# Kernel tuning notes

Hardware: AMD Instinct MI355X
Metric: run time of the kernel (lower is better)

The kernel has to match this reference:

```python
import jax, jax.numpy as jnp
import numpy as np

B, S, D, H, OUT = 512, 200, 64, 512, 1
EPS = 1e-5  # torch LayerNorm default


def ln(x, g, b, axes=-1):
    m = x.mean(axis=axes, keepdims=True)
    v = ((x - m) ** 2).mean(axis=axes, keepdims=True)
    return (x - m) * jax.lax.rsqrt(v + EPS) * g + b


def lstm_layer(xs, W_ih, b_ih, W_hh, b_hh, g_ih, be_ih, g_hh, be_hh, g_ho, be_ho):
    # xs: (S, B, in_dim) -> (S, B, H)
    nb = xs.shape[1]
    def step(carry, x_t):
        h, c = carry
        gates = ln(x_t @ W_ih.T + b_ih, g_ih, be_ih) + ln(h @ W_hh.T + b_hh, g_hh, be_hh)
        i, f, g, o = jnp.split(gates, 4, axis=-1)
        c_new = jax.nn.sigmoid(f) * c + jax.nn.sigmoid(i) * jnp.tanh(g)
        h_new = jax.nn.sigmoid(o) * ln(jnp.tanh(c_new), g_ho, be_ho)
        return (h_new, c_new), h_new
    init = (jnp.zeros((nb, H), xs.dtype), jnp.zeros((nb, H), xs.dtype))
    _, hs = jax.lax.scan(step, init, xs)
    return hs


def setup_inputs() -> dict:
    key = jax.random.key(0)
    ks = iter(jax.random.split(key, 16))
    scale = 0.02
    def rn(shape):
        return jax.random.normal(next(ks), shape, jnp.float32) * scale
    inp = {"x": jax.random.normal(next(ks), (B, S, D), jnp.float32)}
    inp["ln1_g"] = jnp.ones((S, D), jnp.float32)
    inp["ln1_b"] = jnp.zeros((S, D), jnp.float32)
    for l, ind in ((0, D), (1, H)):
        inp[f"W_ih{l}"] = rn((4 * H, ind)); inp[f"b_ih{l}"] = jnp.zeros((4 * H,), jnp.float32)
        inp[f"W_hh{l}"] = rn((4 * H, H));  inp[f"b_hh{l}"] = jnp.zeros((4 * H,), jnp.float32)
        inp[f"g_ih{l}"] = jnp.ones((4 * H,), jnp.float32); inp[f"be_ih{l}"] = jnp.zeros((4 * H,), jnp.float32)
        inp[f"g_hh{l}"] = jnp.ones((4 * H,), jnp.float32); inp[f"be_hh{l}"] = jnp.zeros((4 * H,), jnp.float32)
        inp[f"g_ho{l}"] = jnp.ones((H,), jnp.float32);     inp[f"be_ho{l}"] = jnp.zeros((H,), jnp.float32)
    inp["Wd1"] = rn((H // 4, H));      inp["bd1"] = jnp.zeros((H // 4,), jnp.float32)
    inp["Wd2"] = rn((H // 8, H // 4)); inp["bd2"] = jnp.zeros((H // 8,), jnp.float32)
    inp["Wd3"] = rn((H // 16, H // 8)); inp["bd3"] = jnp.zeros((H // 16,), jnp.float32)
    inp["Wd4"] = rn((OUT, H // 16));   inp["bd4"] = jnp.zeros((OUT,), jnp.float32)
    return inp


def _forward(x, ln1_g, ln1_b,
             W_ih0, b_ih0, W_hh0, b_hh0, g_ih0, be_ih0, g_hh0, be_hh0, g_ho0, be_ho0,
             W_ih1, b_ih1, W_hh1, b_hh1, g_ih1, be_ih1, g_hh1, be_hh1, g_ho1, be_ho1,
             Wd1, bd1, Wd2, bd2, Wd3, bd3, Wd4, bd4):
    # ln1 normalizes jointly over (seq_len, input_dim)
    x = ln(x, ln1_g, ln1_b, axes=(-2, -1))
    xs = jnp.transpose(x, (1, 0, 2))  # (S, B, D)
    hs = lstm_layer(xs, W_ih0, b_ih0, W_hh0, b_hh0, g_ih0, be_ih0, g_hh0, be_hh0, g_ho0, be_ho0)
    hs = lstm_layer(hs, W_ih1, b_ih1, W_hh1, b_hh1, g_ih1, be_ih1, g_hh1, be_hh1, g_ho1, be_ho1)
    h_last = hs[-1]  # (B, H): last_num=1, eval-mode dropout is identity
    z = jax.nn.relu(h_last @ Wd1.T + bd1)
    z = jax.nn.relu(z @ Wd2.T + bd2)
    z = jax.nn.relu(z @ Wd3.T + bd3)
    return z @ Wd4.T + bd4  # (B, OUT)


def reference(x, ln1_g, ln1_b,
              W_ih0, b_ih0, W_hh0, b_hh0, g_ih0, be_ih0, g_hh0, be_hh0, g_ho0, be_ho0,
              W_ih1, b_ih1, W_hh1, b_hh1, g_ih1, be_ih1, g_hh1, be_hh1, g_ho1, be_ho1,
              Wd1, bd1, Wd2, bd2, Wd3, bd3, Wd4, bd4):
    return _forward(x, ln1_g, ln1_b,
                    W_ih0, b_ih0, W_hh0, b_hh0, g_ih0, be_ih0, g_hh0, be_hh0, g_ho0, be_ho0,
                    W_ih1, b_ih1, W_hh1, b_hh1, g_ih1, be_ih1, g_hh1, be_hh1, g_ho1, be_ho1,
                    Wd1, bd1, Wd2, bd2, Wd3, bd3, Wd4, bd4)
```

## Files before the change

kernel.cpp:

```cpp
#include <hip/hip_runtime.h>
#include <math.h>

#define BATCH 512
#define SEQ   200
#define DIN   64
#define HID   512
#define GW    2048
#define EPS   1e-5f
#define NREG  4

typedef _Float16 half_t;
typedef half_t half8 __attribute__((ext_vector_type(8)));
typedef float  f32x4  __attribute__((ext_vector_type(4)));
typedef float  f32x16 __attribute__((ext_vector_type(16)));

#define WN0 (2048*64)
#define WN1 (2048*512)
#define WTOT (WN0 + 3*WN1)
#define XFRAG ((size_t)SEQ*16*4*512)

__device__ __forceinline__ float sigf(float x){ return 1.0f/(1.0f+expf(-x)); }

__device__ __forceinline__ void block_reduce4(float&a,float&b,float&c,float&d,float* red){
  #pragma unroll
  for(int o=32;o;o>>=1){
    a+=__shfl_down(a,o); b+=__shfl_down(b,o);
    c+=__shfl_down(c,o); d+=__shfl_down(d,o);
  }
  const int lane = threadIdx.x & 63, wid = threadIdx.x>>6;
  if(lane==0){ red[wid*4+0]=a; red[wid*4+1]=b; red[wid*4+2]=c; red[wid*4+3]=d; }
  __syncthreads();
  a = red[0]+red[4]+red[8]+red[12];
  b = red[1]+red[5]+red[9]+red[13];
  c = red[2]+red[6]+red[10]+red[14];
  d = red[3]+red[7]+red[11]+red[15];
  __syncthreads();
}

__global__ __launch_bounds__(256) void ln1_stats(const float* __restrict__ x,
                                                 float* __restrict__ mu,
                                                 float* __restrict__ rs){
  const int b = blockIdx.x;
  const float* xb = x + (size_t)b*SEQ*DIN;
  float s=0, ss=0, d=0, e=0;
  for (int i=threadIdx.x; i<SEQ*DIN; i+=256){ float v=xb[i]; s+=v; ss+=v*v; }
  __shared__ float red[16];
  block_reduce4(s,ss,d,e,red);
  if (threadIdx.x==0){
    float m = s*(1.0f/(SEQ*DIN));
    mu[b] = m;
    rs[b] = rsqrtf(ss*(1.0f/(SEQ*DIN)) - m*m + EPS);
  }
}

__global__ __launch_bounds__(256) void wsplit(
    const float* __restrict__ W0, const float* __restrict__ W1,
    const float* __restrict__ W2, const float* __restrict__ W3,
    half_t* __restrict__ Wh, half_t* __restrict__ Wl)
{
  int i = blockIdx.x*256 + threadIdx.x;
  if (i >= WTOT) return;
  const float* src; int off, Kd;
  if (i < WN0){ src=W0; off=i; Kd=DIN; }
  else {
    int r = (i-WN0)/WN1; off = (i-WN0) - r*WN1; Kd=HID;
    src = (r==0)?W1:((r==1)?W2:W3);
  }
  const int C = Kd>>5;
  int j  = off & 7;
  int l  = (off>>3) & 63;
  int ks = (off>>9) & 1;
  int nf = (off>>10) & 1;
  int pc = off>>11;
  int c  = pc & (C-1);
  int p  = pc >> (Kd==DIN ? 1 : 4);
  int n  = p*64 + nf*32 + (l&31);
  int k  = c*32 + ks*16 + (l>>5)*8 + j;
  float v = src[(size_t)n*Kd + k];
  half_t h = (half_t)v;
  Wh[i] = h;
  Wl[i] = (half_t)(v - (float)h);
}

__global__ __launch_bounds__(256) void xprep(
    const float* __restrict__ x, const float* __restrict__ g1, const float* __restrict__ b1,
    const float* __restrict__ mu, const float* __restrict__ rs,
    half_t* __restrict__ xh, half_t* __restrict__ xl)
{
  size_t i = (size_t)blockIdx.x*256 + threadIdx.x;
  if (i >= XFRAG) return;
  int j   = (int)(i & 7);
  int l   = (int)((i>>3) & 63);
  int c   = (int)((i>>9) & 3);
  int mch = (int)((i>>11) & 15);
  int t   = (int)(i>>15);
  int b   = mch*32 + (l&31);
  int k   = c*16 + ((l>>5)<<3) + j;
  float v = (x[(size_t)b*(SEQ*DIN) + t*DIN + k] - mu[b]) * rs[b]
            * g1[t*DIN+k] + b1[t*DIN+k];
  half_t h = (half_t)v;
  xh[i] = h;
  xl[i] = (half_t)(v - (float)h);
}

__global__ __launch_bounds__(256, 1) void tick_mm64(
    const half_t* __restrict__ xh, const half_t* __restrict__ xl,
    const half_t* __restrict__ h0fh, const half_t* __restrict__ h0fl,
    const half_t* __restrict__ h1fh, const half_t* __restrict__ h1fl,
    const half_t* __restrict__ Wh, const half_t* __restrict__ Wl,
    float* __restrict__ G, int t)
{
  const int bi   = blockIdx.x;
  const int xcd  = bi & 7;
  const int slot = bi >> 3;
  const int z    = slot & 3;
  const int y    = (slot >> 2) & 3;
  const int x    = xcd*2 + (slot >> 4);

  const int tid  = threadIdx.x;
  const int lane = tid & 63;
  const int w    = tid >> 6;
  const int ln31 = lane & 31;

  const int mch0 = y*4 + (w>>1)*2;
  const int p    = x*2 + (w&1);
  const int wn0  = p*64;

  const half_t* Bh = Wh + WN0; const half_t* Bl = Wl + WN0;
  int Kd = HID;
  if (z==0){ Bh=Wh; Bl=Wl; Kd=DIN; }
  else if (z==2){ Bh=Wh+WN0+WN1; Bl=Wl+WN0+WN1; }
  else if (z==3){ Bh=Wh+WN0+2*WN1; Bl=Wl+WN0+2*WN1; }

  const int C32 = Kd >> 5;
  const int C16 = Kd >> 4;

  const half_t* Bph = Bh + (size_t)p*C32*2048 + lane*8;
  const half_t* Bpl = Bl + (size_t)p*C32*2048 + lane*8;

  const int tq = (t < SEQ) ? t : (SEQ-1);
  const half_t *Aph0,*Apl0,*Aph1,*Apl1;
  if (z==0){
    const size_t xb = ((size_t)tq*16 + mch0)*2048 + lane*8;
    Aph0 = xh + xb; Aph1 = xh + xb + 2048;
    Apl0 = xl + xb; Apl1 = xl + xb + 2048;
  } else {
    const half_t* FAh = (z==3) ? h1fh : h0fh;
    const half_t* FAl = (z==3) ? h1fl : h0fl;
    const size_t ab = (size_t)mch0*16384 + lane*8;
    Aph0 = FAh + ab; Aph1 = FAh + ab + 16384;
    Apl0 = FAl + ab; Apl1 = FAl + ab + 16384;
  }

  f32x16 acc00 = {0.f,0.f,0.f,0.f,0.f,0.f,0.f,0.f,0.f,0.f,0.f,0.f,0.f,0.f,0.f,0.f};
  f32x16 acc01 = acc00, acc10 = acc00, acc11 = acc00;

  struct F { half8 ah0,al0,ah1,al1,bh0,bh1,bl0,bl1; };
  auto loadF = [&](int c)->F{
    F f;
    const size_t ao = (size_t)c*512;
    f.ah0 = *(const half8*)(Aph0 + ao);
    f.al0 = *(const half8*)(Apl0 + ao);
    f.ah1 = *(const half8*)(Aph1 + ao);
    f.al1 = *(const half8*)(Apl1 + ao);
    const size_t bo = (size_t)(c>>1)*2048 + (size_t)(c&1)*512;
    f.bh0 = *(const half8*)(Bph + bo);
    f.bh1 = *(const half8*)(Bph + bo + 1024);
    f.bl0 = *(const half8*)(Bpl + bo);
    f.bl1 = *(const half8*)(Bpl + bo + 1024);
    return f;
  };
  auto mmstep = [&](const F& f){
    acc00 = __builtin_amdgcn_mfma_f32_32x32x16_f16(f.ah0, f.bh0, acc00, 0,0,0);
    acc01 = __builtin_amdgcn_mfma_f32_32x32x16_f16(f.ah0, f.bh1, acc01, 0,0,0);
    acc10 = __builtin_amdgcn_mfma_f32_32x32x16_f16(f.ah1, f.bh0, acc10, 0,0,0);
    acc11 = __builtin_amdgcn_mfma_f32_32x32x16_f16(f.ah1, f.bh1, acc11, 0,0,0);
    acc00 = __builtin_amdgcn_mfma_f32_32x32x16_f16(f.al0, f.bh0, acc00, 0,0,0);
    acc01 = __builtin_amdgcn_mfma_f32_32x32x16_f16(f.al0, f.bh1, acc01, 0,0,0);
    acc10 = __builtin_amdgcn_mfma_f32_32x32x16_f16(f.al1, f.bh0, acc10, 0,0,0);
    acc11 = __builtin_amdgcn_mfma_f32_32x32x16_f16(f.al1, f.bh1, acc11, 0,0,0);
    acc00 = __builtin_amdgcn_mfma_f32_32x32x16_f16(f.ah0, f.bl0, acc00, 0,0,0);
    acc01 = __builtin_amdgcn_mfma_f32_32x32x16_f16(f.ah0, f.bl1, acc01, 0,0,0);
    acc10 = __builtin_amdgcn_mfma_f32_32x32x16_f16(f.ah1, f.bl0, acc10, 0,0,0);
    acc11 = __builtin_amdgcn_mfma_f32_32x32x16_f16(f.ah1, f.bl1, acc11, 0,0,0);
  };

  F f0 = loadF(0);
  F f1 = loadF(1);
  for (int c=0; c<C16; c+=2){
    F f2, f3;
    if (c+2 < C16){ f2 = loadF(c+2); f3 = loadF(c+3); }
    mmstep(f0);
    mmstep(f1);
    f0 = f2; f1 = f3;
  }

  float* Gr = G + (size_t)z*BATCH*GW;
  const int rbase = (lane>>5)<<2;
  #pragma unroll
  for (int reg=0; reg<16; reg++){
    const int row = (reg&3) + ((reg>>2)<<3) + rbase;
    const int m0 = mch0*32 + row;
    const int m1 = m0 + 32;
    __builtin_nontemporal_store(acc00[reg], &Gr[(size_t)m0*GW + wn0 + ln31]);
    __builtin_nontemporal_store(acc01[reg], &Gr[(size_t)m0*GW + wn0 + 32 + ln31]);
    __builtin_nontemporal_store(acc10[reg], &Gr[(size_t)m1*GW + wn0 + ln31]);
    __builtin_nontemporal_store(acc11[reg], &Gr[(size_t)m1*GW + wn0 + 32 + ln31]);
  }
}

__global__ __launch_bounds__(256) void tick_update(
    const float* __restrict__ G,
    const float* __restrict__ b_ih0, const float* __restrict__ b_hh0,
    const float* __restrict__ b_ih1, const float* __restrict__ b_hh1,
    const float* __restrict__ g_ih0, const float* __restrict__ be_ih0,
    const float* __restrict__ g_hh0, const float* __restrict__ be_hh0,
    const float* __restrict__ g_ho0, const float* __restrict__ be_ho0,
    const float* __restrict__ g_ih1, const float* __restrict__ be_ih1,
    const float* __restrict__ g_hh1, const float* __restrict__ be_hh1,
    const float* __restrict__ g_ho1, const float* __restrict__ be_ho1,
    float* __restrict__ h0, float* __restrict__ c0,
    float* __restrict__ h1, float* __restrict__ c1,
    half_t* __restrict__ h0fh, half_t* __restrict__ h0fl,
    half_t* __restrict__ h1fh, half_t* __restrict__ h1fl, int t)
{
  const int layer = blockIdx.x >> 9;
  const int b = blockIdx.x & 511;
  if (layer==0 && t>=SEQ) return;
  if (layer==1 && t==0)   return;

  const float *GA,*GB,*bA,*bB,*gA,*beA,*gB,*beB,*gH,*bH;
  float *cs,*hs; half_t *hfx,*lfx;
  const size_t rb = (size_t)b*GW;
  if (layer==0){
    GA = G + rb;
    GB = G + (size_t)1*BATCH*GW + rb;
    bA=b_ih0; bB=b_hh0;
    gA=g_ih0; beA=be_ih0; gB=g_hh0; beB=be_hh0; gH=g_ho0; bH=be_ho0;
    cs = c0 + b*HID; hs = nullptr; hfx = h0fh; lfx = h0fl;
  } else {
    GA = G + (size_t)2*BATCH*GW + rb;
    GB = G + (size_t)3*BATCH*GW + rb;
    bA=b_ih1; bB=b_hh1;
    gA=g_ih1; beA=be_ih1; gB=g_hh1; beB=be_hh1; gH=g_ho1; bH=be_ho1;
    cs = c1 + b*HID; hs = (t==SEQ) ? (h1 + b*HID) : nullptr; hfx = h1fh; lfx = h1fl;
  }

  const int tid = threadIdx.x;
  __shared__ float red[16];
  __shared__ __align__(16) float GS[2*GW];
  __shared__ float su[HID];
  __shared__ float so[HID];

  float sa=0, ssa=0, sb=0, ssb=0;
  for (int i=tid*4; i<GW; i+=1024){
    f32x4 va = __builtin_nontemporal_load((const f32x4*)(GA+i));
    va += *(const f32x4*)(bA+i);
    *(f32x4*)(GS+i) = va;
    f32x4 vb = __builtin_nontemporal_load((const f32x4*)(GB+i));
    vb += *(const f32x4*)(bB+i);
    *(f32x4*)(GS+GW+i) = vb;
    #pragma unroll
    for (int q=0;q<4;q++){
      sa += va[q]; ssa += va[q]*va[q];
      sb += vb[q]; ssb += vb[q]*vb[q];
    }
  }
  block_reduce4(sa,ssa,sb,ssb,red);
  const float ma = sa*(1.0f/GW);
  const float ra = rsqrtf(ssa*(1.0f/GW) - ma*ma + EPS);
  const float mb = sb*(1.0f/GW);
  const float rb_ = rsqrtf(ssb*(1.0f/GW) - mb*mb + EPS);

  float s_u=0, s_uu=0;
  for (int j=tid;j<HID;j+=256){
    float iv = ((GS[j      ]-ma)*ra*gA[j      ]+beA[j      ]) + ((GS[GW+j      ]-mb)*rb_*gB[j      ]+beB[j      ]);
    float fv = ((GS[j+  HID]-ma)*ra*gA[j+  HID]+beA[j+  HID]) + ((GS[GW+j+  HID]-mb)*rb_*gB[j+  HID]+beB[j+  HID]);
    float gv = ((GS[j+2*HID]-ma)*ra*gA[j+2*HID]+beA[j+2*HID]) + ((GS[GW+j+2*HID]-mb)*rb_*gB[j+2*HID]+beB[j+2*HID]);
    float ov = ((GS[j+3*HID]-ma)*ra*gA[j+3*HID]+beA[j+3*HID]) + ((GS[GW+j+3*HID]-mb)*rb_*gB[j+3*HID]+beB[j+3*HID]);
    float cn = sigf(fv)*cs[j] + sigf(iv)*tanhf(gv);
    cs[j] = cn;
    float u = tanhf(cn);
    su[j] = u; so[j] = sigf(ov);
    s_u += u; s_uu += u*u;
  }
  float d3=0,d4=0;
  block_reduce4(s_u,s_uu,d3,d4,red);
  const float mu_u = s_u*(1.0f/HID);
  const float ru   = rsqrtf(s_uu*(1.0f/HID) - mu_u*mu_u + EPS);

  const size_t fbase = ((size_t)(b>>5)*32)*512 + (size_t)(b&31)*8;
  for (int j=tid;j<HID;j+=256){
    float v = so[j] * ((su[j]-mu_u)*ru*gH[j] + bH[j]);
    if (hs) hs[j] = v;
    half_t hv = (half_t)v;
    half_t lv = (half_t)(v - (float)hv);
    const size_t fi = fbase + (size_t)(j>>4)*512 + (size_t)((j>>3)&1)*256 + (j&7);
    hfx[fi] = hv;
    lfx[fi] = lv;
  }
}

__global__ __launch_bounds__(256) void head_kernel(
    const float* __restrict__ h1,
    const float* __restrict__ Wd1, const float* __restrict__ bd1,
    const float* __restrict__ Wd2, const float* __restrict__ bd2,
    const float* __restrict__ Wd3, const float* __restrict__ bd3,
    const float* __restrict__ Wd4, const float* __restrict__ bd4,
    float* __restrict__ out)
{
  const int b = blockIdx.x;
  __shared__ float hv[HID];
  __shared__ float z1[128];
  __shared__ float z2[64];
  __shared__ float z3[32];
  const int tid = threadIdx.x;
  for (int i=tid;i<HID;i+=256) hv[i]=h1[(size_t)b*HID+i];
  __syncthreads();
  if (tid<128){
    float acc=bd1[tid]; const float* w=Wd1+(size_t)tid*512;
    for(int k=0;k<512;k++) acc+=hv[k]*w[k];
    z1[tid]=fmaxf(acc,0.f);
  }
  __syncthreads();
  if (tid<64){
    float acc=bd2[tid]; const float* w=Wd2+(size_t)tid*128;
    for(int k=0;k<128;k++) acc+=z1[k]*w[k];
    z2[tid]=fmaxf(acc,0.f);
  }
  __syncthreads();
  if (tid<32){
    float acc=bd3[tid]; const float* w=Wd3+(size_t)tid*64;
    for(int k=0;k<64;k++) acc+=z2[k]*w[k];
    z3[tid]=fmaxf(acc,0.f);
  }
  __syncthreads();
  if (tid==0){
    float acc=bd4[0];
    for(int k=0;k<32;k++) acc+=z3[k]*Wd4[k];
    out[b]=acc;
  }
}

extern "C" void kernel_launch(void* const* d_in, const int* in_sizes, int n_in,
                              void* d_out, int out_size, void* d_ws, size_t ws_size,
                              hipStream_t stream) {
  const float* x      = (const float*)d_in[0];
  const float* ln1_g  = (const float*)d_in[1];
  const float* ln1_b  = (const float*)d_in[2];
  const float* W_ih0  = (const float*)d_in[3];
  const float* b_ih0  = (const float*)d_in[4];
  const float* W_hh0  = (const float*)d_in[5];
  const float* b_hh0  = (const float*)d_in[6];
  const float* g_ih0  = (const float*)d_in[7];
  const float* be_ih0 = (const float*)d_in[8];
  const float* g_hh0  = (const float*)d_in[9];
  const float* be_hh0 = (const float*)d_in[10];
  const float* g_ho0  = (const float*)d_in[11];
  const float* be_ho0 = (const float*)d_in[12];
  const float* W_ih1  = (const float*)d_in[13];
  const float* b_ih1  = (const float*)d_in[14];
  const float* W_hh1  = (const float*)d_in[15];
  const float* b_hh1  = (const float*)d_in[16];
  const float* g_ih1  = (const float*)d_in[17];
  const float* be_ih1 = (const float*)d_in[18];
  const float* g_hh1  = (const float*)d_in[19];
  const float* be_hh1 = (const float*)d_in[20];
  const float* g_ho1  = (const float*)d_in[21];
  const float* be_ho1 = (const float*)d_in[22];
  const float* Wd1    = (const float*)d_in[23];
  const float* bd1    = (const float*)d_in[24];
  const float* Wd2    = (const float*)d_in[25];
  const float* bd2    = (const float*)d_in[26];
  const float* Wd3    = (const float*)d_in[27];
  const float* bd3    = (const float*)d_in[28];
  const float* Wd4    = (const float*)d_in[29];
  const float* bd4    = (const float*)d_in[30];
  float* out = (float*)d_out;

  float* ws = (float*)d_ws;
  float* G  = ws;
  float* h0 = G  + NREG*(size_t)BATCH*GW;
  float* c0 = h0 + (size_t)BATCH*HID;
  float* h1 = c0 + (size_t)BATCH*HID;
  float* c1 = h1 + (size_t)BATCH*HID;
  half_t* h0fh = (half_t*)(c1 + (size_t)BATCH*HID);
  half_t* h0fl = h0fh + (size_t)BATCH*HID;
  half_t* h1fh = h0fl + (size_t)BATCH*HID;
  half_t* h1fl = h1fh + (size_t)BATCH*HID;
  float* mu = (float*)(h1fl + (size_t)BATCH*HID);
  float* rs = mu + BATCH;
  half_t* Wh = (half_t*)(rs + BATCH);
  half_t* Wl = Wh + (size_t)WTOT;
  half_t* xh = Wl + (size_t)WTOT;
  half_t* xl = xh + XFRAG;

  (void)hipMemsetAsync(h0, 0, 4*(size_t)BATCH*HID*4 + 4*(size_t)BATCH*HID*2, stream);

  ln1_stats<<<BATCH, 256, 0, stream>>>(x, mu, rs);
  wsplit<<<(WTOT+255)/256, 256, 0, stream>>>(W_ih0, W_hh0, W_ih1, W_hh1, Wh, Wl);
  xprep<<<(int)((XFRAG+255)/256), 256, 0, stream>>>(x, ln1_g, ln1_b, mu, rs, xh, xl);

  for (int t = 0; t <= SEQ; ++t) {
    tick_mm64<<<dim3(256), 256, 0, stream>>>(xh, xl,
        h0fh, h0fl, h1fh, h1fl, Wh, Wl, G, t);
    tick_update<<<dim3(1024), 256, 0, stream>>>(G,
        b_ih0, b_hh0, b_ih1, b_hh1,
        g_ih0, be_ih0, g_hh0, be_hh0, g_ho0, be_ho0,
        g_ih1, be_ih1, g_hh1, be_hh1, g_ho1, be_ho1,
        h0, c0, h1, c1, h0fh, h0fl, h1fh, h1fl, t);
  }
  head_kernel<<<BATCH, 256, 0, stream>>>(h1, Wd1, bd1, Wd2, bd2, Wd3, bd3, Wd4, bd4, out);
}
```

Measured before the change: 5.724 ms.

## Stage GEMM operands through LDS with async global_load_lds double buffering

Rewrites the per-tick MFMA GEMM so A and B fragments are loaded with global_load_lds into a double-buffered shared-memory tile, with waves split into A-loaders and B-loaders. Each wave then reads its fragments from LDS, which lets the two waves that share A and B tiles reuse them instead of each fetching from global memory. The cost is two barriers per K-chunk and hand-tuned vmcnt waits that depend on the per-wave load count, which is a correctness risk.

```diff
diff --git a/kernel.cpp b/kernel.cpp
--- a/kernel.cpp
+++ b/kernel.cpp
@@ -20,6 +20,18 @@
 #define XFRAG ((size_t)SEQ*16*4*512)
 
 __device__ __forceinline__ float sigf(float x){ return 1.0f/(1.0f+expf(-x)); }
+
+__device__ __forceinline__ void gload16(const half_t* g, half_t* l){
+  __builtin_amdgcn_global_load_lds(
+      (const __attribute__((address_space(1))) void*)g,
+      (__attribute__((address_space(3))) void*)l, 16, 0, 0);
+}
+
+__device__ __forceinline__ void barf(){
+  asm volatile("" ::: "memory");
+  __builtin_amdgcn_s_barrier();
+  asm volatile("" ::: "memory");
+}
 
 __device__ __forceinline__ void block_reduce4(float&a,float&b,float&c,float&d,float* red){
   #pragma unroll
@@ -110,6 +122,8 @@
     const half_t* __restrict__ Wh, const half_t* __restrict__ Wl,
     float* __restrict__ G, int t)
 {
+  __shared__ half_t sbuf[2*16384];
+
   const int bi   = blockIdx.x;
   const int xcd  = bi & 7;
   const int slot = bi >> 3;
@@ -126,73 +140,93 @@
   const int p    = x*2 + (w&1);
   const int wn0  = p*64;
 
-  const half_t* Bh = Wh + WN0; const half_t* Bl = Wl + WN0;
+  const half_t* BHb = Wh + WN0; const half_t* BLb = Wl + WN0;
   int Kd = HID;
-  if (z==0){ Bh=Wh; Bl=Wl; Kd=DIN; }
-  else if (z==2){ Bh=Wh+WN0+WN1; Bl=Wl+WN0+WN1; }
-  else if (z==3){ Bh=Wh+WN0+2*WN1; Bl=Wl+WN0+2*WN1; }
+  if (z==0){ BHb=Wh; BLb=Wl; Kd=DIN; }
+  else if (z==2){ BHb=Wh+WN0+WN1; BLb=Wl+WN0+WN1; }
+  else if (z==3){ BHb=Wh+WN0+2*WN1; BLb=Wl+WN0+2*WN1; }
 
   const int C32 = Kd >> 5;
   const int C16 = Kd >> 4;
 
-  const half_t* Bph = Bh + (size_t)p*C32*2048 + lane*8;
-  const half_t* Bpl = Bl + (size_t)p*C32*2048 + lane*8;
-
   const int tq = (t < SEQ) ? t : (SEQ-1);
-  const half_t *Aph0,*Apl0,*Aph1,*Apl1;
-  if (z==0){
-    const size_t xb = ((size_t)tq*16 + mch0)*2048 + lane*8;
-    Aph0 = xh + xb; Aph1 = xh + xb + 2048;
-    Apl0 = xl + xb; Apl1 = xl + xb + 2048;
-  } else {
-    const half_t* FAh = (z==3) ? h1fh : h0fh;
-    const half_t* FAl = (z==3) ? h1fl : h0fl;
-    const size_t ab = (size_t)mch0*16384 + lane*8;
-    Aph0 = FAh + ab; Aph1 = FAh + ab + 16384;
-    Apl0 = FAl + ab; Apl1 = FAl + ab + 16384;
-  }
+  const half_t *AHb, *ALb;
+  if (z==0){ AHb = xh + (size_t)tq*32768; ALb = xl + (size_t)tq*32768; }
+  else if (z==3){ AHb = h1fh; ALb = h1fl; }
+  else { AHb = h0fh; ALb = h0fl; }
+
+  auto stage = [&](int s){
+    half_t* dst = sbuf + (size_t)(s&1)*16384;
+    if (w < 2){
+      #pragma unroll
+      for (int q=0;q<2;q++){
+        const int mci = w*2+q;
+        const size_t abase = ((size_t)(y*4+mci)*C16 + 2*s)*512;
+        #pragma unroll
+        for (int pl=0;pl<2;pl++){
+          const half_t* src = (pl? ALb : AHb) + abase + lane*8;
+          half_t* d = dst + (mci*2+pl)*1024;
+          gload16(src,       d);
+          gload16(src + 512, d + 512);
+        }
+      }
+    } else {
+      const int ph = w-2;
+      const size_t bbase = ((size_t)(x*2+ph)*C32 + s)*2048;
+      #pragma unroll
+      for (int pl=0;pl<2;pl++){
+        const half_t* src = (pl? BLb : BHb) + bbase + lane*8;
+        half_t* d = dst + 8192 + (ph*2+pl)*2048;
+        #pragma unroll
+        for (int i=0;i<4;i++)
+          gload16(src + i*512, d + i*512);
+      }
+    }
+  };
 
   f32x16 acc00 = {0.f,0.f,0.f,0.f,0.f,0.f,0.f,0.f,0.f,0.f,0.f,0.f,0.f,0.f,0.f,0.f};
   f32x16 acc01 = acc00, acc10 = acc00, acc11 = acc00;
 
-  struct F { half8 ah0,al0,ah1,al1,bh0,bh1,bl0,bl1; };
-  auto loadF = [&](int c)->F{
-    F f;
-    const size_t ao = (size_t)c*512;
-    f.ah0 = *(const half8*)(Aph0 + ao);
-    f.al0 = *(const half8*)(Apl0 + ao);
-    f.ah1 = *(const half8*)(Aph1 + ao);
-    f.al1 = *(const half8*)(Apl1 + ao);
-    const size_t bo = (size_t)(c>>1)*2048 + (size_t)(c&1)*512;
-    f.bh0 = *(const half8*)(Bph + bo);
-    f.bh1 = *(const half8*)(Bph + bo + 1024);
-    f.bl0 = *(const half8*)(Bpl + bo);
-    f.bl1 = *(const half8*)(Bpl + bo + 1024);
-    return f;
+  const int mh = w>>1, pw = w&1;
+  auto compute = [&](const half_t* buf, int ks){
+    const half_t* Ab = buf;
+    const half_t* Bb = buf + 8192;
+    half8 ah0 = *(const half8*)(Ab + ((mh*2+0)*2+0)*1024 + ks*512 + lane*8);
+    half8 al0 = *(const half8*)(Ab + ((mh*2+0)*2+1)*1024 + ks*512 + lane*8);
+    half8 ah1 = *(const half8*)(Ab + ((mh*2+1)*2+0)*1024 + ks*512 + lane*8);
+    half8 al1 = *(const half8*)(Ab + ((mh*2+1)*2+1)*1024 + ks*512 + lane*8);
+    half8 bh0 = *(const half8*)(Bb + ((pw*2+0)*4 + 0 + ks)*512 + lane*8);
+    half8 bh1 = *(const half8*)(Bb + ((pw*2+0)*4 + 2 + ks)*512 + lane*8);
+    half8 bl0 = *(const half8*)(Bb + ((pw*2+1)*4 + 0 + ks)*512 + lane*8);
+    half8 bl1 = *(const half8*)(Bb + ((pw*2+1)*4 + 2 + ks)*512 + lane*8);
+    acc00 = __builtin_amdgcn_mfma_f32_32x32x16_f16(ah0, bh0, acc00, 0,0,0);
+    acc01 = __builtin_amdgcn_mfma_f32_32x32x16_f16(ah0, bh1, acc01, 0,0,0);
+    acc10 = __builtin_amdgcn_mfma_f32_32x32x16_f16(ah1, bh0, acc10, 0,0,0);
+    acc11 = __builtin_amdgcn_mfma_f32_32x32x16_f16(ah1, bh1, acc11, 0,0,0);
+    acc00 = __builtin_amdgcn_mfma_f32_32x32x16_f16(al0, bh0, acc00, 0,0,0);
+    acc01 = __builtin_amdgcn_mfma_f32_32x32x16_f16(al0, bh1, acc01, 0,0,0);
+    acc10 = __builtin_amdgcn_mfma_f32_32x32x16_f16(al1, bh0, acc10, 0,0,0);
+    acc11 = __builtin_amdgcn_mfma_f32_32x32x16_f16(al1, bh1, acc11, 0,0,0);
+    acc00 = __builtin_amdgcn_mfma_f32_32x32x16_f16(ah0, bl0, acc00, 0,0,0);
+    acc01 = __builtin_amdgcn_mfma_f32_32x32x16_f16(ah0, bl1, acc01, 0,0,0);
+    acc10 = __builtin_amdgcn_mfma_f32_32x32x16_f16(ah1, bl0, acc10, 0,0,0);
+    acc11 = __builtin_amdgcn_mfma_f32_32x32x16_f16(ah1, bl1, acc11, 0,0,0);
   };
-  auto mmstep = [&](const F& f){
-    acc00 = __builtin_amdgcn_mfma_f32_32x32x16_f16(f.ah0, f.bh0, acc00, 0,0,0);
-    acc01 = __builtin_amdgcn_mfma_f32_32x32x16_f16(f.ah0, f.bh1, acc01, 0,0,0);
-    acc10 = __builtin_amdgcn_mfma_f32_32x32x16_f16(f.ah1, f.bh0, acc10, 0,0,0);
-    acc11 = __builtin_amdgcn_mfma_f32_32x32x16_f16(f.ah1, f.bh1, acc11, 0,0,0);
-    acc00 = __builtin_amdgcn_mfma_f32_32x32x16_f16(f.al0, f.bh0, acc00, 0,0,0);
-    acc01 = __builtin_amdgcn_mfma_f32_32x32x16_f16(f.al0, f.bh1, acc01, 0,0,0);
-    acc10 = __builtin_amdgcn_mfma_f32_32x32x16_f16(f.al1, f.bh0, acc10, 0,0,0);
-    acc11 = __builtin_amdgcn_mfma_f32_32x32x16_f16(f.al1, f.bh1, acc11, 0,0,0);
-    acc00 = __builtin_amdgcn_mfma_f32_32x32x16_f16(f.ah0, f.bl0, acc00, 0,0,0);
-    acc01 = __builtin_amdgcn_mfma_f32_32x32x16_f16(f.ah0, f.bl1, acc01, 0,0,0);
-    acc10 = __builtin_amdgcn_mfma_f32_32x32x16_f16(f.ah1, f.bl0, acc10, 0,0,0);
-    acc11 = __builtin_amdgcn_mfma_f32_32x32x16_f16(f.ah1, f.bl1, acc11, 0,0,0);
-  };
-
-  F f0 = loadF(0);
-  F f1 = loadF(1);
-  for (int c=0; c<C16; c+=2){
-    F f2, f3;
-    if (c+2 < C16){ f2 = loadF(c+2); f3 = loadF(c+3); }
-    mmstep(f0);
-    mmstep(f1);
-    f0 = f2; f1 = f3;
+
+  stage(0);
+  for (int s=0; s<C32; ++s){
+    if (s+1 < C32){
+      stage(s+1);
+      asm volatile("s_waitcnt vmcnt(8)" ::: "memory");
+    } else {
+      asm volatile("s_waitcnt vmcnt(0)" ::: "memory");
+    }
+    __builtin_amdgcn_sched_barrier(0);
+    barf();
+    const half_t* buf = sbuf + (size_t)(s&1)*16384;
+    compute(buf, 0);
+    compute(buf, 1);
+    barf();
   }
 
   float* Gr = G + (size_t)z*BATCH*GW;
```

Measured after the change: 5.498 ms. -3.9%, faster.
